# Kernel optimization log

Measured on AMD Instinct MI355X. Metric: run time of the kernel, lower is better.

## Reference

```python
import jax, jax.numpy as jnp
import numpy as np

N_NODES = 100000
N_EDGES = 1000000
M_DIM = 4
HID = 64
N_GRAPHS = 64


def setup_inputs() -> dict:
    key = jax.random.key(0)
    ks = jax.random.split(key, 16)
    x = jax.random.normal(ks[0], (N_NODES, 1, M_DIM), dtype=jnp.float32)
    edge_index = jax.random.randint(ks[1], (2, N_EDGES), 0, N_NODES, dtype=jnp.int64)
    batch = jnp.sort(jax.random.randint(ks[2], (N_NODES,), 0, N_GRAPHS, dtype=jnp.int64))
    def lin(k, out_c, in_c):
        bound = 1.0 / np.sqrt(in_c)
        return jax.random.uniform(k, (out_c, in_c), jnp.float32, -bound, bound)
    inp = {"x": x, "edge_index": edge_index, "batch": batch}
    inp["W1l"] = lin(ks[3], HID, 1); inp["b1l"] = jnp.zeros((HID,), jnp.float32)
    inp["W1r"] = lin(ks[4], HID, 1)
    inp["W2l"] = lin(ks[5], HID, HID); inp["b2l"] = jnp.zeros((HID,), jnp.float32)
    inp["W2r"] = lin(ks[6], HID, HID)
    inp["W3l"] = lin(ks[7], HID, HID); inp["b3l"] = jnp.zeros((HID,), jnp.float32)
    inp["W3r"] = lin(ks[8], HID, HID)
    inp["Wlin"] = lin(ks[9], 1, HID); inp["blin"] = jnp.zeros((1,), jnp.float32)
    return inp


def _sage_conv(x, src, dst, Wl, bl, Wr):
    # x: [N, F, M]; mean aggregation over in-edges, then lin_l/lin_r GEMMs.
    N, F, M = x.shape
    msg = x[src]  # [E, F, M] gather
    s = jax.ops.segment_sum(msg, dst, num_segments=N)
    cnt = jax.ops.segment_sum(jnp.ones((src.shape[0],), x.dtype), dst, num_segments=N)
    agg = s / jnp.maximum(cnt, 1.0)[:, None, None]  # [N, F, M]
    C = Wl.shape[0]
    # torch .view(N*M, F) on contiguous [N,F,M] == row-major reshape (mixes F and M)
    h = (agg.reshape(N * M, F) @ Wl.T + bl).reshape(N, C, M)
    h = h + (x.reshape(N * M, F) @ Wr.T).reshape(N, C, M)
    return h


def reference(x, edge_index, batch, W1l, b1l, W1r, W2l, b2l, W2r, W3l, b3l, W3r, Wlin, blin):
    src, dst = edge_index[0], edge_index[1]
    h = jax.nn.relu(_sage_conv(x, src, dst, W1l, b1l, W1r))
    h = jax.nn.relu(_sage_conv(h, src, dst, W2l, b2l, W2r))
    h = jax.nn.relu(_sage_conv(h, src, dst, W3l, b3l, W3r))
    # new_global_mean_pool: scatter-mean over nodes -> [B, HID, M]
    sums = jax.ops.segment_sum(h, batch, num_segments=N_GRAPHS)
    cnts = jax.ops.segment_sum(jnp.ones((h.shape[0],), h.dtype), batch, num_segments=N_GRAPHS)
    pooled = sums / jnp.maximum(cnts, 1.0)[:, None, None]
    # dropout in eval mode == identity
    B, F, M = pooled.shape
    z = (pooled.reshape(B * M, F) @ Wlin.T + blin).reshape(B, M)
    return jax.nn.sigmoid(z).mean(axis=1)  # [B]
```

## Files before the change

### kernel.cpp

```cpp
#include <hip/hip_runtime.h>
#include <math.h>

#define TPB 256

typedef unsigned short ushort_t;
typedef unsigned char uchar_t;
typedef __attribute__((ext_vector_type(8))) short short8v;
typedef __attribute__((ext_vector_type(4))) float f32x4;
typedef __attribute__((ext_vector_type(8))) unsigned short ushort8;
typedef __attribute__((ext_vector_type(4))) int intv4;

__device__ __forceinline__ unsigned short f2b(float f) {
  union { float f; unsigned int i; } c; c.f = f;
  unsigned int x = c.i;
  x += 0x7FFFu + ((x >> 16) & 1u);
  return (unsigned short)(x >> 16);
}

__device__ __forceinline__ short8v fp8x8_to_bf16(const uchar_t* p) {
  uint2 u = *(const uint2*)p;
  auto p0 = __builtin_amdgcn_cvt_pk_f32_fp8(u.x, false);
  auto p1 = __builtin_amdgcn_cvt_pk_f32_fp8(u.x, true);
  auto p2 = __builtin_amdgcn_cvt_pk_f32_fp8(u.y, false);
  auto p3 = __builtin_amdgcn_cvt_pk_f32_fp8(u.y, true);
  ushort8 o;
  o[0] = f2b(p0[0]); o[1] = f2b(p0[1]); o[2] = f2b(p1[0]); o[3] = f2b(p1[1]);
  o[4] = f2b(p2[0]); o[5] = f2b(p2[1]); o[6] = f2b(p3[0]); o[7] = f2b(p3[1]);
  union { ushort8 a; short8v b; } c; c.a = o; return c.b;
}

__global__ void k_histg(const int* __restrict__ dst, int* deg,
                        const int* __restrict__ batch, int* gcnt, int E, int N) {
  int t = blockIdx.x * TPB + threadIdx.x;
  if (t < E) atomicAdd(&deg[__builtin_nontemporal_load(dst + t)], 1);
  int n0 = t * 16;
  if (n0 < N) {
    int n1 = min(n0 + 16, N);
    int cur = batch[n0];
    int c = 0;
    for (int n = n0; n < n1; ++n) {
      int b = batch[n];
      if (b != cur) { atomicAdd(&gcnt[cur], c); cur = b; c = 0; }
      ++c;
    }
    atomicAdd(&gcnt[cur], c);
  }
}

__global__ void k_scan1(const int* __restrict__ deg, int* rp, int* bsum, int N) {
  __shared__ int s[TPB];
  int t = threadIdx.x;
  int i = blockIdx.x * TPB + t;
  int v = (i < N) ? ((deg[i] + 7) & ~7) : 0;
  s[t] = v;
  __syncthreads();
  for (int d = 1; d < TPB; d <<= 1) {
    int u = (t >= d) ? s[t - d] : 0;
    __syncthreads();
    s[t] += u;
    __syncthreads();
  }
  if (i < N) rp[i] = s[t] - v;
  if (t == TPB - 1) bsum[blockIdx.x] = s[t];
}

__global__ void k_scan2(const int* bsum, int* boff, int nb) {
  __shared__ int s[1024];
  int t = threadIdx.x;
  int v = (t < nb) ? bsum[t] : 0;
  s[t] = v;
  __syncthreads();
  for (int d = 1; d < 1024; d <<= 1) {
    int u = (t >= d) ? s[t - d] : 0;
    __syncthreads();
    s[t] += u;
    __syncthreads();
  }
  if (t < nb) boff[t] = s[t] - v;
}

__global__ void k_scan3(int* rp, const int* __restrict__ boff, const int* __restrict__ bsum,
                        int* cursor, int N, int nb) {
  int i = blockIdx.x * TPB + threadIdx.x;
  if (i < N) {
    int v = rp[i] + boff[i >> 8];
    rp[i] = v;
    cursor[i] = v;
  } else if (i == N) {
    rp[N] = boff[nb - 1] + bsum[nb - 1];
  }
}

__global__ void k_fill(const intv4* __restrict__ src4, const intv4* __restrict__ dst4,
                       int* cursor, int* __restrict__ csr, int E4, int E) {
  int q = blockIdx.x * TPB + threadIdx.x;
  if (q >= E4) return;
  intv4 d = __builtin_nontemporal_load(dst4 + q);
  intv4 s = __builtin_nontemporal_load(src4 + q);
  int base = q * 4;
#pragma unroll
  for (int j = 0; j < 4; ++j) {
    if (base + j < E) {
      int p = atomicAdd(&cursor[d[j]], 1);
      __builtin_nontemporal_store(s[j], csr + p);
    }
  }
}

__global__ void k_cvtw(const float* __restrict__ s0, const float* __restrict__ s1,
                       const float* __restrict__ s2, const float* __restrict__ s3,
                       ushort_t* d0, ushort_t* d1, ushort_t* d2, ushort_t* d3,
                       uchar_t* zr0, int n) {
  int i = blockIdx.x * TPB + threadIdx.x;
  if (i < n) { d0[i] = f2b(s0[i]); d1[i] = f2b(s1[i]); d2[i] = f2b(s2[i]); d3[i] = f2b(s3[i]); }
  if (blockIdx.x == 0 && threadIdx.x < 64) ((int*)zr0)[threadIdx.x] = 0;
}

__global__ void k_agg1(const float4* __restrict__ x, const int* __restrict__ rp,
                       const int* __restrict__ deg, const int* __restrict__ cursor,
                       int* __restrict__ csr, float4* __restrict__ agg1, int N) {
  int n = blockIdx.x * TPB + threadIdx.x;
  if (n >= N) return;
  int b = rp[n], e = rp[n + 1];
  float4 a = make_float4(0.f, 0.f, 0.f, 0.f);
  for (int i = b; i < e; i += 8) {
    int4 c0 = *(const int4*)(csr + i);
    int4 c1 = *(const int4*)(csr + i + 4);
    int id[8] = {c0.x, c0.y, c0.z, c0.w, c1.x, c1.y, c1.z, c1.w};
#pragma unroll
    for (int j = 0; j < 8; ++j) {
      unsigned idx = min((unsigned)id[j], (unsigned)(N - 1));
      float m = ((unsigned)id[j] < (unsigned)N) ? 1.f : 0.f;
      float4 v = x[idx];
      a.x += v.x * m; a.y += v.y * m; a.z += v.z * m; a.w += v.w * m;
    }
  }
  int d = deg[n];
  float inv = (d > 0) ? 1.f / (float)d : 0.f;
  a.x *= inv; a.y *= inv; a.z *= inv; a.w *= inv;
  agg1[n] = a;
  int c = cursor[n];
  for (int p2 = c; p2 < e; ++p2) csr[p2] = N;
}

__global__ __launch_bounds__(256) void k_gemm(
    const uchar_t* __restrict__ hIn8,
    const float* __restrict__ xf, const float* __restrict__ agg1f,
    const float* __restrict__ W1l, const float* __restrict__ b1l,
    const float* __restrict__ W1r,
    const ushort_t* __restrict__ Wlb, const ushort_t* __restrict__ Wrb,
    const float* __restrict__ bias,
    uchar_t* __restrict__ Yl8, uchar_t* __restrict__ Yr8, int rows) {
  int t = threadIdx.x;
  int wave = t >> 6, lane = t & 63;
  int g = lane >> 4, l15 = lane & 15;
  int r0 = blockIdx.x * 64 + wave * 16;
  int r = r0 + l15;

  short8v af0, af1;
  if (hIn8) {
    const uchar_t* hrow = hIn8 + (size_t)r * 64;
    af0 = fp8x8_to_bf16(hrow + g * 8);
    af1 = fp8x8_to_bf16(hrow + 32 + g * 8);
  } else {
    float sA = agg1f[r], sX = xf[r];
    ushort8 o0, o1;
#pragma unroll
    for (int k = 0; k < 8; ++k) {
      int c0 = g * 8 + k, c1 = 32 + g * 8 + k;
      o0[k] = f2b(fmaxf(sA * W1l[c0] + b1l[c0] + sX * W1r[c0], 0.f));
      o1[k] = f2b(fmaxf(sA * W1l[c1] + b1l[c1] + sX * W1r[c1], 0.f));
    }
    union { ushort8 a; short8v b; } u0, u1;
    u0.a = o0; u1.a = o1;
    af0 = u0.b; af1 = u1.b;
  }

#pragma unroll
  for (int c = 0; c < 4; ++c) {
    const ushort_t* wl = Wlb + (size_t)(c * 16 + l15) * 64;
    const ushort_t* wr = Wrb + (size_t)(c * 16 + l15) * 64;
    short8v bl0 = *(const short8v*)(wl + g * 8);
    short8v bl1 = *(const short8v*)(wl + 32 + g * 8);
    short8v br0 = *(const short8v*)(wr + g * 8);
    short8v br1 = *(const short8v*)(wr + 32 + g * 8);
    float bv = bias[c * 16 + l15];
    f32x4 accl = (f32x4){0.f, 0.f, 0.f, 0.f};
    f32x4 accr = (f32x4){bv, bv, bv, bv};
    accl = __builtin_amdgcn_mfma_f32_16x16x32_bf16(af0, bl0, accl, 0, 0, 0);
    accl = __builtin_amdgcn_mfma_f32_16x16x32_bf16(af1, bl1, accl, 0, 0, 0);
    accr = __builtin_amdgcn_mfma_f32_16x16x32_bf16(af0, br0, accr, 0, 0, 0);
    accr = __builtin_amdgcn_mfma_f32_16x16x32_bf16(af1, br1, accr, 0, 0, 0);
#pragma unroll
    for (int i = 0; i < 4; ++i) {
      size_t off = (size_t)(r0 + g * 4 + i) * 64 + c * 16 + l15;
      Yl8[off] = (uchar_t)(__builtin_amdgcn_cvt_pk_fp8_f32(accl[i], accl[i], 0u, false) & 0xFF);
      Yr8[off] = (uchar_t)(__builtin_amdgcn_cvt_pk_fp8_f32(accr[i], accr[i], 0u, false) & 0xFF);
    }
  }
}

#define ADD8(IDX) { \
    uint2 v = *(const uint2*)(base + ((size_t)(unsigned)(IDX) << 8)); \
    auto q0 = __builtin_amdgcn_cvt_pk_f32_fp8(v.x, false); \
    auto q1 = __builtin_amdgcn_cvt_pk_f32_fp8(v.x, true);  \
    auto q2 = __builtin_amdgcn_cvt_pk_f32_fp8(v.y, false); \
    auto q3 = __builtin_amdgcn_cvt_pk_f32_fp8(v.y, true);  \
    acc[0] += q0[0]; acc[1] += q0[1]; acc[2] += q1[0]; acc[3] += q1[1]; \
    acc[4] += q2[0]; acc[5] += q2[1]; acc[6] += q3[0]; acc[7] += q3[1]; }

__global__ __launch_bounds__(256) void k_gather(
    const uchar_t* __restrict__ Yl8, const uchar_t* __restrict__ Yr8,
    const int* __restrict__ rp, const int* __restrict__ deg, const int* __restrict__ csr,
    uchar_t* __restrict__ hOut8, float* __restrict__ pooled,
    const int* __restrict__ batch, int N) {
  __shared__ float ps[1024];
  int tid = blockIdx.x * TPB + threadIdx.x;
  int n = tid >> 5, s = tid & 31;
  bool alive = (n < N);

  float acc[8];
#pragma unroll
  for (int j = 0; j < 8; ++j) acc[j] = 0.f;

  float h[8];
#pragma unroll
  for (int j = 0; j < 8; ++j) h[j] = 0.f;

  if (alive) {
    int b = rp[n], e = rp[n + 1];
    const uchar_t* base = Yl8 + s * 8;
    for (int i = b; i < e; i += 8) {
      int4 c0 = *(const int4*)(csr + i);
      int4 c1 = *(const int4*)(csr + i + 4);
      ADD8(c0.x) ADD8(c0.y) ADD8(c0.z) ADD8(c0.w)
      ADD8(c1.x) ADD8(c1.y) ADD8(c1.z) ADD8(c1.w)
    }
    int d = deg[n];
    float inv = (d > 0) ? 1.f / (float)d : 0.f;
    uint2 yr = *(const uint2*)(Yr8 + (size_t)n * 256 + s * 8);
    auto y0 = __builtin_amdgcn_cvt_pk_f32_fp8(yr.x, false);
    auto y1 = __builtin_amdgcn_cvt_pk_f32_fp8(yr.x, true);
    auto y2 = __builtin_amdgcn_cvt_pk_f32_fp8(yr.y, false);
    auto y3 = __builtin_amdgcn_cvt_pk_f32_fp8(yr.y, true);
    h[0] = fmaxf(acc[0] * inv + y0[0], 0.f);
    h[1] = fmaxf(acc[1] * inv + y0[1], 0.f);
    h[2] = fmaxf(acc[2] * inv + y1[0], 0.f);
    h[3] = fmaxf(acc[3] * inv + y1[1], 0.f);
    h[4] = fmaxf(acc[4] * inv + y2[0], 0.f);
    h[5] = fmaxf(acc[5] * inv + y2[1], 0.f);
    h[6] = fmaxf(acc[6] * inv + y3[0], 0.f);
    h[7] = fmaxf(acc[7] * inv + y3[1], 0.f);
  }

  if (hOut8) {
    if (alive) {
      unsigned int w0 = __builtin_amdgcn_cvt_pk_fp8_f32(h[0], h[1], 0u, false);
      w0 = __builtin_amdgcn_cvt_pk_fp8_f32(h[2], h[3], w0, true);
      unsigned int w1 = __builtin_amdgcn_cvt_pk_fp8_f32(h[4], h[5], 0u, false);
      w1 = __builtin_amdgcn_cvt_pk_fp8_f32(h[6], h[7], w1, true);
      uint2 st; st.x = w0; st.y = w1;
      *(uint2*)(hOut8 + (size_t)n * 256 + s * 8) = st;
    }
    return;
  }

  int nb0 = (blockIdx.x * TPB) >> 5;
  int nlast = min(nb0 + 7, N - 1);
  int bF = batch[nb0], bL = batch[nlast];
  if (bF == bL) {
    int wave = threadIdx.x >> 6;
    int lane = threadIdx.x & 63;
#pragma unroll
    for (int j = 0; j < 8; ++j) h[j] += __shfl_xor(h[j], 32);
    if (lane < 32) {
#pragma unroll
      for (int j = 0; j < 8; ++j) ps[wave * 256 + s * 8 + j] = h[j];
    }
    __syncthreads();
    int t = threadIdx.x;
    if (t < 256) {
      float v = ps[t] + ps[256 + t] + ps[512 + t] + ps[768 + t];
      atomicAdd(&pooled[bF * 256 + t], v);
    }
  } else {
    if (alive) {
      int bb = batch[n];
#pragma unroll
      for (int j = 0; j < 8; ++j)
        atomicAdd(&pooled[bb * 256 + s * 8 + j], h[j]);
    }
  }
}

__global__ void k_final(const float* __restrict__ pooled, const int* __restrict__ gcnt,
                        const float* __restrict__ Wlin, const float* __restrict__ blin,
                        float* __restrict__ out, int B) {
  int t = blockIdx.x * TPB + threadIdx.x;
  int b = t >> 2, j = t & 3;
  if (b >= B) return;
  float inv = 1.f / fmaxf((float)gcnt[b], 1.f);
  float s = blin[0];
  const float* p = pooled + b * 256 + j * 64;
#pragma unroll
  for (int f = 0; f < 64; ++f) s += p[f] * inv * Wlin[f];
  float z = 1.f / (1.f + expf(-s));
  z += __shfl_xor(z, 1);
  z += __shfl_xor(z, 2);
  if (j == 0) out[b] = 0.25f * z;
}

extern "C" void kernel_launch(void* const* d_in, const int* in_sizes, int n_in,
                              void* d_out, int out_size, void* d_ws, size_t ws_size,
                              hipStream_t stream) {
  const float* x   = (const float*)d_in[0];
  const int* edge  = (const int*)d_in[1];
  const int* batch = (const int*)d_in[2];
  const float* W1l = (const float*)d_in[3];
  const float* b1l = (const float*)d_in[4];
  const float* W1r = (const float*)d_in[5];
  const float* W2l = (const float*)d_in[6];
  const float* b2l = (const float*)d_in[7];
  const float* W2r = (const float*)d_in[8];
  const float* W3l = (const float*)d_in[9];
  const float* b3l = (const float*)d_in[10];
  const float* W3r = (const float*)d_in[11];
  const float* Wlin = (const float*)d_in[12];
  const float* blin = (const float*)d_in[13];
  float* out = (float*)d_out;

  const int N = in_sizes[0] / 4;
  const int E = in_sizes[1] / 2;
  const int B = out_size;
  const int rows = 4 * N;

  const int* srcA = edge;
  const int* dstA = edge + E;

  char* p = (char*)d_ws;
  auto carve = [&](size_t bytes) -> void* {
    void* r = (void*)p;
    p += (bytes + 255) & ~(size_t)255;
    return r;
  };
  char* zstart = p;
  int* deg     = (int*)carve((size_t)N * 4);
  int* gcnt    = (int*)carve((size_t)B * 4);
  float* pooled = (float*)carve((size_t)B * 256 * 4);
  size_t zlen  = (size_t)(p - zstart);
  int* rp      = (int*)carve((size_t)(N + 1) * 4);
  int* cursor  = (int*)carve((size_t)N * 4);
  int* bsum    = (int*)carve(4096);
  int* boff    = (int*)carve(4096);
  int* csr     = (int*)carve(((size_t)E + 8 * (size_t)N) * 4);
  float* agg1  = (float*)carve((size_t)N * 4 * 4);
  ushort_t* Wb2l = (ushort_t*)carve(4096 * 2);
  ushort_t* Wb2r = (ushort_t*)carve(4096 * 2);
  ushort_t* Wb3l = (ushort_t*)carve(4096 * 2);
  ushort_t* Wb3r = (ushort_t*)carve(4096 * 2);
  uchar_t* Yl8 = (uchar_t*)carve(((size_t)N + 1) * 256);
  uchar_t* Yr8 = (uchar_t*)carve((size_t)N * 256);
  uchar_t* h8  = (uchar_t*)carve((size_t)N * 256);
  (void)ws_size; (void)n_in;

  hipMemsetAsync(zstart, 0, zlen, stream);

  int nbScan = (N + TPB - 1) / TPB;
  int E4 = (E + 3) / 4;

  k_histg<<<(E + TPB - 1) / TPB, TPB, 0, stream>>>(dstA, deg, batch, gcnt, E, N);
  k_cvtw<<<16, TPB, 0, stream>>>(W2l, W2r, W3l, W3r, Wb2l, Wb2r, Wb3l, Wb3r,
                                 Yl8 + (size_t)N * 256, 4096);
  k_scan1<<<nbScan, TPB, 0, stream>>>(deg, rp, bsum, N);
  k_scan2<<<1, 1024, 0, stream>>>(bsum, boff, nbScan);
  k_scan3<<<(N + 1 + TPB - 1) / TPB, TPB, 0, stream>>>(rp, boff, bsum, cursor, N, nbScan);
  k_fill<<<(E4 + TPB - 1) / TPB, TPB, 0, stream>>>((const intv4*)srcA, (const intv4*)dstA,
                                                   cursor, csr, E4, E);

  k_agg1<<<(N + TPB - 1) / TPB, TPB, 0, stream>>>((const float4*)x, rp, deg, cursor,
                                                  csr, (float4*)agg1, N);

  int nbGemm = (rows + 63) / 64;
  int nbGather = ((size_t)N * 32 + TPB - 1) / TPB;

  k_gemm<<<nbGemm, TPB, 0, stream>>>((const uchar_t*)nullptr, x, agg1, W1l, b1l, W1r,
                                     Wb2l, Wb2r, b2l, Yl8, Yr8, rows);
  k_gather<<<nbGather, TPB, 0, stream>>>(Yl8, Yr8, rp, deg, csr, h8,
                                         (float*)nullptr, batch, N);

  k_gemm<<<nbGemm, TPB, 0, stream>>>(h8, x, agg1, W1l, b1l, W1r,
                                     Wb3l, Wb3r, b3l, Yl8, Yr8, rows);
  k_gather<<<nbGather, TPB, 0, stream>>>(Yl8, Yr8, rp, deg, csr, (uchar_t*)nullptr,
                                         pooled, batch, N);

  k_final<<<(B * 4 + TPB - 1) / TPB, TPB, 0, stream>>>(pooled, gcnt, Wlin, blin, out, B);
}
```

Baseline: 436.0 us.

## Widen gather to 16 lanes per node with 16-byte loads; simplify CSR fill

The gather kernel now assigns 16 threads per node instead of 32. Each thread reads 16 fp8 bytes per neighbor row with a uint4 load, which halves the number of index loads and loop iterations per node and issues wider memory transactions. The pooling reduction is adjusted with an extra shuffle step and 16-node block spans. Separately, the CSR fill and histogram kernels go back from 4-wide nontemporal vector accesses to plain scalar per-edge accesses. This spends more registers per thread and gives less parallelism per node in exchange for fewer instructions.

New measurement: 420.3 us. 1.04x faster.

```diff
diff --git a/kernel.cpp b/kernel.cpp
--- a/kernel.cpp
+++ b/kernel.cpp
@@ -8,7 +8,6 @@
 typedef __attribute__((ext_vector_type(8))) short short8v;
 typedef __attribute__((ext_vector_type(4))) float f32x4;
 typedef __attribute__((ext_vector_type(8))) unsigned short ushort8;
-typedef __attribute__((ext_vector_type(4))) int intv4;
 
 __device__ __forceinline__ unsigned short f2b(float f) {
   union { float f; unsigned int i; } c; c.f = f;
@@ -32,7 +31,7 @@
 __global__ void k_histg(const int* __restrict__ dst, int* deg,
                         const int* __restrict__ batch, int* gcnt, int E, int N) {
   int t = blockIdx.x * TPB + threadIdx.x;
-  if (t < E) atomicAdd(&deg[__builtin_nontemporal_load(dst + t)], 1);
+  if (t < E) atomicAdd(&deg[dst[t]], 1);
   int n0 = t * 16;
   if (n0 < N) {
     int n1 = min(n0 + 16, N);
@@ -91,19 +90,12 @@
   }
 }
 
-__global__ void k_fill(const intv4* __restrict__ src4, const intv4* __restrict__ dst4,
-                       int* cursor, int* __restrict__ csr, int E4, int E) {
-  int q = blockIdx.x * TPB + threadIdx.x;
-  if (q >= E4) return;
-  intv4 d = __builtin_nontemporal_load(dst4 + q);
-  intv4 s = __builtin_nontemporal_load(src4 + q);
-  int base = q * 4;
-#pragma unroll
-  for (int j = 0; j < 4; ++j) {
-    if (base + j < E) {
-      int p = atomicAdd(&cursor[d[j]], 1);
-      __builtin_nontemporal_store(s[j], csr + p);
-    }
+__global__ void k_fill(const int* __restrict__ src, const int* __restrict__ dst,
+                       int* cursor, int* __restrict__ csr, int E) {
+  int e = blockIdx.x * TPB + threadIdx.x;
+  if (e < E) {
+    int p = atomicAdd(&cursor[dst[e]], 1);
+    csr[p] = src[e];
   }
 }
 
@@ -200,14 +192,20 @@
   }
 }
 
-#define ADD8(IDX) { \
-    uint2 v = *(const uint2*)(base + ((size_t)(unsigned)(IDX) << 8)); \
+#define ADD16(IDX) { \
+    uint4 v = *(const uint4*)(base + ((size_t)(unsigned)(IDX) << 8)); \
     auto q0 = __builtin_amdgcn_cvt_pk_f32_fp8(v.x, false); \
     auto q1 = __builtin_amdgcn_cvt_pk_f32_fp8(v.x, true);  \
     auto q2 = __builtin_amdgcn_cvt_pk_f32_fp8(v.y, false); \
     auto q3 = __builtin_amdgcn_cvt_pk_f32_fp8(v.y, true);  \
-    acc[0] += q0[0]; acc[1] += q0[1]; acc[2] += q1[0]; acc[3] += q1[1]; \
-    acc[4] += q2[0]; acc[5] += q2[1]; acc[6] += q3[0]; acc[7] += q3[1]; }
+    auto q4 = __builtin_amdgcn_cvt_pk_f32_fp8(v.z, false); \
+    auto q5 = __builtin_amdgcn_cvt_pk_f32_fp8(v.z, true);  \
+    auto q6 = __builtin_amdgcn_cvt_pk_f32_fp8(v.w, false); \
+    auto q7 = __builtin_amdgcn_cvt_pk_f32_fp8(v.w, true);  \
+    acc[0] += q0[0];  acc[1] += q0[1];  acc[2] += q1[0];  acc[3] += q1[1];  \
+    acc[4] += q2[0];  acc[5] += q2[1];  acc[6] += q3[0];  acc[7] += q3[1];  \
+    acc[8] += q4[0];  acc[9] += q4[1];  acc[10] += q5[0]; acc[11] += q5[1]; \
+    acc[12] += q6[0]; acc[13] += q6[1]; acc[14] += q7[0]; acc[15] += q7[1]; }
 
 __global__ __launch_bounds__(256) void k_gather(
     const uchar_t* __restrict__ Yl8, const uchar_t* __restrict__ Yr8,
@@ -216,41 +214,52 @@
     const int* __restrict__ batch, int N) {
   __shared__ float ps[1024];
   int tid = blockIdx.x * TPB + threadIdx.x;
-  int n = tid >> 5, s = tid & 31;
+  int n = tid >> 4, s = tid & 15;
   bool alive = (n < N);
 
-  float acc[8];
-#pragma unroll
-  for (int j = 0; j < 8; ++j) acc[j] = 0.f;
-
-  float h[8];
-#pragma unroll
-  for (int j = 0; j < 8; ++j) h[j] = 0.f;
+  float acc[16];
+#pragma unroll
+  for (int j = 0; j < 16; ++j) acc[j] = 0.f;
+  float h[16];
+#pragma unroll
+  for (int j = 0; j < 16; ++j) h[j] = 0.f;
 
   if (alive) {
     int b = rp[n], e = rp[n + 1];
-    const uchar_t* base = Yl8 + s * 8;
+    const uchar_t* base = Yl8 + s * 16;
     for (int i = b; i < e; i += 8) {
       int4 c0 = *(const int4*)(csr + i);
       int4 c1 = *(const int4*)(csr + i + 4);
-      ADD8(c0.x) ADD8(c0.y) ADD8(c0.z) ADD8(c0.w)
-      ADD8(c1.x) ADD8(c1.y) ADD8(c1.z) ADD8(c1.w)
+      ADD16(c0.x) ADD16(c0.y) ADD16(c0.z) ADD16(c0.w)
+      ADD16(c1.x) ADD16(c1.y) ADD16(c1.z) ADD16(c1.w)
     }
     int d = deg[n];
     float inv = (d > 0) ? 1.f / (float)d : 0.f;
-    uint2 yr = *(const uint2*)(Yr8 + (size_t)n * 256 + s * 8);
+    uint4 yr = *(const uint4*)(Yr8 + (size_t)n * 256 + s * 16);
     auto y0 = __builtin_amdgcn_cvt_pk_f32_fp8(yr.x, false);
     auto y1 = __builtin_amdgcn_cvt_pk_f32_fp8(yr.x, true);
     auto y2 = __builtin_amdgcn_cvt_pk_f32_fp8(yr.y, false);
     auto y3 = __builtin_amdgcn_cvt_pk_f32_fp8(yr.y, true);
-    h[0] = fmaxf(acc[0] * inv + y0[0], 0.f);
-    h[1] = fmaxf(acc[1] * inv + y0[1], 0.f);
-    h[2] = fmaxf(acc[2] * inv + y1[0], 0.f);
-    h[3] = fmaxf(acc[3] * inv + y1[1], 0.f);
-    h[4] = fmaxf(acc[4] * inv + y2[0], 0.f);
-    h[5] = fmaxf(acc[5] * inv + y2[1], 0.f);
-    h[6] = fmaxf(acc[6] * inv + y3[0], 0.f);
-    h[7] = fmaxf(acc[7] * inv + y3[1], 0.f);
+    auto y4 = __builtin_amdgcn_cvt_pk_f32_fp8(yr.z, false);
+    auto y5 = __builtin_amdgcn_cvt_pk_f32_fp8(yr.z, true);
+    auto y6 = __builtin_amdgcn_cvt_pk_f32_fp8(yr.w, false);
+    auto y7 = __builtin_amdgcn_cvt_pk_f32_fp8(yr.w, true);
+    h[0]  = fmaxf(acc[0]  * inv + y0[0], 0.f);
+    h[1]  = fmaxf(acc[1]  * inv + y0[1], 0.f);
+    h[2]  = fmaxf(acc[2]  * inv + y1[0], 0.f);
+    h[3]  = fmaxf(acc[3]  * inv + y1[1], 0.f);
+    h[4]  = fmaxf(acc[4]  * inv + y2[0], 0.f);
+    h[5]  = fmaxf(acc[5]  * inv + y2[1], 0.f);
+    h[6]  = fmaxf(acc[6]  * inv + y3[0], 0.f);
+    h[7]  = fmaxf(acc[7]  * inv + y3[1], 0.f);
+    h[8]  = fmaxf(acc[8]  * inv + y4[0], 0.f);
+    h[9]  = fmaxf(acc[9]  * inv + y4[1], 0.f);
+    h[10] = fmaxf(acc[10] * inv + y5[0], 0.f);
+    h[11] = fmaxf(acc[11] * inv + y5[1], 0.f);
+    h[12] = fmaxf(acc[12] * inv + y6[0], 0.f);
+    h[13] = fmaxf(acc[13] * inv + y6[1], 0.f);
+    h[14] = fmaxf(acc[14] * inv + y7[0], 0.f);
+    h[15] = fmaxf(acc[15] * inv + y7[1], 0.f);
   }
 
   if (hOut8) {
@@ -259,36 +268,41 @@
       w0 = __builtin_amdgcn_cvt_pk_fp8_f32(h[2], h[3], w0, true);
       unsigned int w1 = __builtin_amdgcn_cvt_pk_fp8_f32(h[4], h[5], 0u, false);
       w1 = __builtin_amdgcn_cvt_pk_fp8_f32(h[6], h[7], w1, true);
-      uint2 st; st.x = w0; st.y = w1;
-      *(uint2*)(hOut8 + (size_t)n * 256 + s * 8) = st;
+      unsigned int w2 = __builtin_amdgcn_cvt_pk_fp8_f32(h[8], h[9], 0u, false);
+      w2 = __builtin_amdgcn_cvt_pk_fp8_f32(h[10], h[11], w2, true);
+      unsigned int w3 = __builtin_amdgcn_cvt_pk_fp8_f32(h[12], h[13], 0u, false);
+      w3 = __builtin_amdgcn_cvt_pk_fp8_f32(h[14], h[15], w3, true);
+      uint4 st; st.x = w0; st.y = w1; st.z = w2; st.w = w3;
+      *(uint4*)(hOut8 + (size_t)n * 256 + s * 16) = st;
     }
     return;
   }
 
-  int nb0 = (blockIdx.x * TPB) >> 5;
-  int nlast = min(nb0 + 7, N - 1);
+  int nb0 = (blockIdx.x * TPB) >> 4;
+  int nlast = min(nb0 + 15, N - 1);
   int bF = batch[nb0], bL = batch[nlast];
   if (bF == bL) {
     int wave = threadIdx.x >> 6;
     int lane = threadIdx.x & 63;
 #pragma unroll
-    for (int j = 0; j < 8; ++j) h[j] += __shfl_xor(h[j], 32);
-    if (lane < 32) {
-#pragma unroll
-      for (int j = 0; j < 8; ++j) ps[wave * 256 + s * 8 + j] = h[j];
+    for (int j = 0; j < 16; ++j) {
+      h[j] += __shfl_xor(h[j], 16);
+      h[j] += __shfl_xor(h[j], 32);
+    }
+    if (lane < 16) {
+#pragma unroll
+      for (int j = 0; j < 16; ++j) ps[wave * 256 + s * 16 + j] = h[j];
     }
     __syncthreads();
     int t = threadIdx.x;
-    if (t < 256) {
-      float v = ps[t] + ps[256 + t] + ps[512 + t] + ps[768 + t];
-      atomicAdd(&pooled[bF * 256 + t], v);
-    }
+    float v = ps[t] + ps[256 + t] + ps[512 + t] + ps[768 + t];
+    atomicAdd(&pooled[bF * 256 + t], v);
   } else {
     if (alive) {
       int bb = batch[n];
 #pragma unroll
-      for (int j = 0; j < 8; ++j)
-        atomicAdd(&pooled[bb * 256 + s * 8 + j], h[j]);
+      for (int j = 0; j < 16; ++j)
+        atomicAdd(&pooled[bb * 256 + s * 16 + j], h[j]);
     }
   }
 }
@@ -366,7 +380,6 @@
   hipMemsetAsync(zstart, 0, zlen, stream);
 
   int nbScan = (N + TPB - 1) / TPB;
-  int E4 = (E + 3) / 4;
 
   k_histg<<<(E + TPB - 1) / TPB, TPB, 0, stream>>>(dstA, deg, batch, gcnt, E, N);
   k_cvtw<<<16, TPB, 0, stream>>>(W2l, W2r, W3l, W3r, Wb2l, Wb2r, Wb3l, Wb3r,
@@ -374,14 +387,13 @@
   k_scan1<<<nbScan, TPB, 0, stream>>>(deg, rp, bsum, N);
   k_scan2<<<1, 1024, 0, stream>>>(bsum, boff, nbScan);
   k_scan3<<<(N + 1 + TPB - 1) / TPB, TPB, 0, stream>>>(rp, boff, bsum, cursor, N, nbScan);
-  k_fill<<<(E4 + TPB - 1) / TPB, TPB, 0, stream>>>((const intv4*)srcA, (const intv4*)dstA,
-                                                   cursor, csr, E4, E);
+  k_fill<<<(E + TPB - 1) / TPB, TPB, 0, stream>>>(srcA, dstA, cursor, csr, E);
 
   k_agg1<<<(N + TPB - 1) / TPB, TPB, 0, stream>>>((const float4*)x, rp, deg, cursor,
                                                   csr, (float4*)agg1, N);
 
   int nbGemm = (rows + 63) / 64;
-  int nbGather = ((size_t)N * 32 + TPB - 1) / TPB;
+  int nbGather = ((size_t)N * 16 + TPB - 1) / TPB;
 
   k_gemm<<<nbGemm, TPB, 0, stream>>>((const uchar_t*)nullptr, x, agg1, W1l, b1l, W1r,
                                      Wb2l, Wb2r, b2l, Yl8, Yr8, rows);
```
